# Performance work log

Hardware: AMD Instinct MI355X
Metric: run time of the kernel (lower is better)

## Reference

```python
import jax, jax.numpy as jnp
import numpy as np

B, T, C, HS = 8, 4096, 1024, 128

def setup_inputs() -> dict:
    key = jax.random.key(0)
    kx, kq, kk, kv = jax.random.split(key, 4)
    x = jax.random.normal(kx, (B, T, C), dtype=jnp.float32)
    # Linear weights stored as [in, out] so projection is x @ W
    Wq = jax.random.normal(kq, (C, HS), dtype=jnp.float32) * (C ** -0.5)
    Wk = jax.random.normal(kk, (C, HS), dtype=jnp.float32) * (C ** -0.5)
    Wv = jax.random.normal(kv, (C, HS), dtype=jnp.float32) * (C ** -0.5)
    return {"x": x, "Wq": Wq, "Wk": Wk, "Wv": Wv}

def reference(x, Wq, Wk, Wv):
    # one head of causal self-attention (dropout=0.0 -> identity)
    q = x @ Wq  # [B,T,HS]
    k = x @ Wk
    v = x @ Wv
    scale = q.shape[-1] ** -0.5
    scores = jnp.einsum('bqd,bkd->bqk', q, k) * scale  # [B,T,T]
    t = q.shape[1]
    causal = jnp.tril(jnp.ones((t, t), dtype=bool))
    scores = jnp.where(causal, scores, jnp.finfo(scores.dtype).min)
    weights = jax.nn.softmax(scores, axis=-1)
    out = jnp.einsum('bqk,bkd->bqd', weights, v)  # [B,T,HS]
    return out
```

## Files before the change

### kernel.cpp

```cpp
#include <hip/hip_runtime.h>
#include <hip/hip_bf16.h>

#define TB 8
#define TT 4096
#define TC 1024
#define THS 128

typedef __bf16 bf16;
typedef __attribute__((ext_vector_type(8))) __bf16 bf16x8;
typedef __attribute__((ext_vector_type(2))) __bf16 bf16x2;
typedef __attribute__((ext_vector_type(4))) float f32x4;
typedef __attribute__((ext_vector_type(16))) float f32x16;

__device__ __forceinline__ unsigned pkbf(float a, float b) {
    bf16x2 t = { (bf16)a, (bf16)b };
    return __builtin_bit_cast(unsigned, t);
}

__device__ __forceinline__ void gload16(const void* g, void* l) {
    __builtin_amdgcn_global_load_lds(
        (const __attribute__((address_space(1))) void*)g,
        (__attribute__((address_space(3))) void*)l, 16, 0, 0);
}

__global__ __launch_bounds__(256) void wt_kernel(const float* __restrict__ Wq,
                                                 const float* __restrict__ Wk,
                                                 const float* __restrict__ Wv,
                                                 bf16* __restrict__ Wt) {
    __shared__ float tile[64][65];
    const int tid = threadIdx.x;
    const int idx = blockIdx.x;
    const int w = idx >> 5;
    const int kt = (idx & 31) >> 1, ntb = idx & 1;
    const int k0 = kt * 64, n0 = ntb * 64;
    const float* W = (w == 0) ? Wq : (w == 1) ? Wk : Wv;
    #pragma unroll
    for (int i = 0; i < 4; i++) {
        int r = (tid >> 4) + i * 16;
        int c4 = (tid & 15) * 4;
        float4 x4 = *reinterpret_cast<const float4*>(&W[(long)(k0 + r) * 128 + n0 + c4]);
        tile[r][c4 + 0] = x4.x; tile[r][c4 + 1] = x4.y;
        tile[r][c4 + 2] = x4.z; tile[r][c4 + 3] = x4.w;
    }
    __syncthreads();
    const int n = tid >> 2, kk = (tid & 3) * 16;
    bf16 o[16];
    #pragma unroll
    for (int j = 0; j < 16; j++) o[j] = (bf16)tile[kk + j][n];
    bf16* dst = &Wt[(long)((w << 7) + n0 + n) * 1024 + k0 + kk];
    *reinterpret_cast<bf16x8*>(dst)     = *reinterpret_cast<bf16x8*>(&o[0]);
    *reinterpret_cast<bf16x8*>(dst + 8) = *reinterpret_cast<bf16x8*>(&o[8]);
}

__global__ __launch_bounds__(512, 4) void qkv_kernel(const float* __restrict__ x,
                                                     const bf16* __restrict__ Wt,
                                                     bf16* __restrict__ Q,
                                                     bf16* __restrict__ K,
                                                     bf16* __restrict__ Vtt) {
    __shared__ __align__(1024) char smem[81920];
    const int tid = threadIdx.x;
    const int wave = tid >> 6, lane = tid & 63;
    const int lr = lane & 15, g = lane >> 4;
    const int qs = wave >> 2, ns = wave & 3;
    const long row0 = (long)blockIdx.x * 64;

    int xOff[2], xL[2];
    #pragma unroll
    for (int i = 0; i < 2; i++) {
        int D = wave * 2048 + i * 1024 + lane * 16;
        int r = D >> 8, c = D & 255;
        xOff[i] = r * 4096 + (c ^ (((r & 7) << 4) ^ (((r >> 3) & 1) << 7)));
        xL[i] = wave * 2048 + i * 1024;
    }
    int wOff[6], wL[6];
    #pragma unroll
    for (int i = 0; i < 6; i++) {
        int D = wave * 6144 + i * 1024 + lane * 16;
        int n = D >> 7, c = D & 127;
        wOff[i] = n * 2048 + (c ^ ((n & 7) << 4));
        wL[i] = wave * 6144 + i * 1024;
    }
    const char* xb = (const char*)x + row0 * 4096;
    const char* wb = (const char*)Wt;

    f32x4 acc[2][6] = {};

    {
        #pragma unroll
        for (int i = 0; i < 2; i++) gload16(xb + xOff[i], smem + xL[i]);
        #pragma unroll
        for (int i = 0; i < 6; i++) gload16(wb + wOff[i], smem + 32768 + wL[i]);
        #pragma unroll
        for (int i = 0; i < 2; i++) gload16(xb + 256 + xOff[i], smem + 16384 + xL[i]);
    }

    #pragma unroll 1
    for (int s = 0; s < 16; s++) {
        if (s < 15) asm volatile("s_waitcnt vmcnt(2)" ::: "memory");
        else        asm volatile("s_waitcnt vmcnt(0)" ::: "memory");
        __builtin_amdgcn_s_barrier();

        const char* xp = smem + (s & 1) * 16384;
        const char* wp = smem + 32768;
        bf16x8 a[2][2];
        #pragma unroll
        for (int ar = 0; ar < 2; ar++) {
            const int r = qs * 32 + ar * 16 + lr;
            const int rs = ((r & 7) << 4) ^ (((r >> 3) & 1) << 7);
            #pragma unroll
            for (int ks = 0; ks < 2; ks++) {
                f32x4 lo  = *reinterpret_cast<const f32x4*>(xp + r * 256 + ((ks * 128 + g * 32) ^ rs));
                f32x4 hi4 = *reinterpret_cast<const f32x4*>(xp + r * 256 + ((ks * 128 + g * 32 + 16) ^ rs));
                uint4 u;
                u.x = pkbf(lo[0], lo[1]);  u.y = pkbf(lo[2], lo[3]);
                u.z = pkbf(hi4[0], hi4[1]); u.w = pkbf(hi4[2], hi4[3]);
                a[ar][ks] = __builtin_bit_cast(bf16x8, u);
            }
        }
        __builtin_amdgcn_s_setprio(1);
        #pragma unroll
        for (int nt = 0; nt < 6; nt++) {
            const int n = ns * 96 + nt * 16 + lr;
            const int nsw = (n & 7) << 4;
            #pragma unroll
            for (int ks = 0; ks < 2; ks++) {
                bf16x8 bfr = *reinterpret_cast<const bf16x8*>(wp + n * 128 + ((ks * 64 + g * 16) ^ nsw));
                #pragma unroll
                for (int ar = 0; ar < 2; ar++)
                    acc[ar][nt] = __builtin_amdgcn_mfma_f32_16x16x32_bf16(a[ar][ks], bfr, acc[ar][nt], 0, 0, 0);
            }
        }
        __builtin_amdgcn_s_setprio(0);
        __builtin_amdgcn_s_barrier();

        if (s + 1 < 16) {
            #pragma unroll
            for (int i = 0; i < 6; i++)
                gload16(wb + (s + 1) * 128 + wOff[i], smem + 32768 + wL[i]);
        }
        if (s + 2 < 16) {
            #pragma unroll
            for (int i = 0; i < 2; i++)
                gload16(xb + (s + 2) * 256 + xOff[i], smem + (s & 1) * 16384 + xL[i]);
        }
    }

    const float qscale = 0.08838834764831845f;
    bf16* ld = (bf16*)smem;
    #pragma unroll 1
    for (int wsel = 0; wsel < 3; wsel++) {
        __syncthreads();
        #pragma unroll
        for (int nt = 0; nt < 6; nt++) {
            const int colbase = ns * 96 + nt * 16;
            if ((colbase >> 7) != wsel) continue;
            const int d = (colbase + lr) & 127;
            #pragma unroll
            for (int ar = 0; ar < 2; ar++)
                #pragma unroll
                for (int r = 0; r < 4; r++) {
                    float val = acc[ar][nt][r];
                    if (wsel == 0) val *= qscale;
                    const int lrow = qs * 32 + ar * 16 + g * 4 + r;
                    ld[lrow * 136 + d] = (bf16)val;
                }
        }
        __syncthreads();
        if (wsel < 2) {
            bf16* dst = (wsel == 0 ? Q : K) + row0 * 128;
            #pragma unroll
            for (int i = 0; i < 2; i++) {
                const int slot = tid + 512 * i;
                const int rr = slot >> 4, c8 = (slot & 15) * 8;
                bf16x8 vv = *reinterpret_cast<const bf16x8*>(&ld[rr * 136 + c8]);
                *reinterpret_cast<bf16x8*>(&dst[rr * 128 + c8]) = vv;
            }
        } else {
            bf16* dst = Vtt + (long)blockIdx.x * 8192;
            #pragma unroll
            for (int i = 0; i < 2; i++) {
                const int slot = tid + 512 * i;
                const int d = slot >> 3, t8 = (slot & 7) * 8;
                bf16x8 vv;
                #pragma unroll
                for (int j = 0; j < 8; j++) vv[j] = ld[(t8 + j) * 136 + d];
                *reinterpret_cast<bf16x8*>(&dst[d * 64 + t8]) = vv;
            }
        }
    }
}

__global__ __launch_bounds__(512, 2) void attn_kernel(const bf16* __restrict__ Q,
                                                      const bf16* __restrict__ K,
                                                      const bf16* __restrict__ Vtt,
                                                      float* __restrict__ out) {
    __shared__ __align__(1024) char smem[131072];
    __shared__ float mlb[6 * 64];
    const int tid = threadIdx.x;
    const int wave = tid >> 6, lane = tid & 63;
    const int c = lane & 31, hi = lane >> 5;
    const int qs = wave >> 2, kvq = wave & 3;
    const int kswz = ((c & 7) << 4) ^ (((c >> 3) & 1) << 7);
    const int vswz = (c & 7) << 4;
    const int v = blockIdx.x >> 3, b = blockIdx.x & 7;
    const long base = (long)b * TT * 128;
    const char* Kb = (const char*)(K + base);
    const char* Vb = (const char*)Vtt + (long)b * (64 * 16384);

    int kOff[4], vOff[4], lOff[4];
    #pragma unroll
    for (int i = 0; i < 4; i++) {
        int D = wave * 4096 + i * 1024 + lane * 16;
        kOff[i] = (D & ~255) | ((D & 255) ^ (((D >> 8) & 7) << 4) ^ (((D >> 11) & 1) << 7));
        vOff[i] = (D & ~127) | ((D & 127) ^ (((D >> 7) & 7) << 4));
        lOff[i] = wave * 4096 + i * 1024;
    }

    #pragma unroll 1
    for (int ph = 0; ph < 2; ph++) {
        const int qt = ph ? 63 - v : v;
        const int nIt = (qt + 2) >> 1;
        const int q0w = qt * 64 + qs * 32;
        const int qa = q0w + c;

        bf16x8 qf[8];
        #pragma unroll
        for (int dw = 0; dw < 8; dw++)
            qf[dw] = *reinterpret_cast<const bf16x8*>(&Q[base + (long)qa * 128 + dw * 16 + hi * 8]);

        f32x16 O[4] = {};
        float m = -__builtin_inff(), l = 0.f;

        {
            #pragma unroll
            for (int i = 0; i < 4; i++) {
                gload16(Kb + kOff[i], smem + lOff[i]);
                gload16(Vb + vOff[i], smem + 65536 + lOff[i]);
            }
            if (nIt > 1) {
                #pragma unroll
                for (int i = 0; i < 4; i++) {
                    gload16(Kb + 32768 + kOff[i], smem + 32768 + lOff[i]);
                    gload16(Vb + 32768 + vOff[i], smem + 98304 + lOff[i]);
                }
            }
        }

        #pragma unroll 1
        for (int it = 0; it < nIt; it++) {
            const int bi = it & 1;
            char* kBuf = smem + bi * 32768;
            char* vBuf = smem + 65536 + bi * 32768;
            if (it + 1 < nIt) asm volatile("s_waitcnt vmcnt(8)" ::: "memory");
            else              asm volatile("s_waitcnt vmcnt(0)" ::: "memory");
            __builtin_amdgcn_s_barrier();

            const int kv0 = it * 128 + kvq * 32;
            if (kv0 <= q0w) {
                const char* kb = kBuf + kvq * 8192;
                const char* vb = vBuf + (kvq >> 1) * 16384;
                const int vcol0 = (kvq & 1) * 64;
                f32x16 S = {};
                __builtin_amdgcn_s_setprio(1);
                #pragma unroll
                for (int dw = 0; dw < 8; dw++) {
                    bf16x8 kf = *reinterpret_cast<const bf16x8*>(
                        kb + c * 256 + ((dw * 32 + hi * 16) ^ kswz));
                    S = __builtin_amdgcn_mfma_f32_32x32x16_bf16(kf, qf[dw], S, 0, 0, 0);
                }
                __builtin_amdgcn_s_setprio(0);
                if (kv0 == q0w) {
                    #pragma unroll
                    for (int i = 0; i < 16; i++) {
                        int kvr = kv0 + (i & 3) + 8 * (i >> 2) + 4 * hi;
                        if (kvr > qa) S[i] = -__builtin_inff();
                    }
                }
                float t8[8];
                #pragma unroll
                for (int i = 0; i < 8; i++) t8[i] = fmaxf(S[i], S[i + 8]);
                float t4a = fmaxf(t8[0], t8[4]), t4b = fmaxf(t8[1], t8[5]);
                float t4c = fmaxf(t8[2], t8[6]), t4d = fmaxf(t8[3], t8[7]);
                float pm = fmaxf(fmaxf(t4a, t4b), fmaxf(t4c, t4d));
                pm = fmaxf(pm, __shfl_xor(pm, 32, 64));
                if (!__all(pm - m <= 8.0f)) {
                    float mn = fmaxf(m, pm);
                    float fr = __expf(m - mn);
                    #pragma unroll
                    for (int dt = 0; dt < 4; dt++) O[dt] = O[dt] * fr;
                    l *= fr;
                    m = mn;
                }
                #pragma unroll
                for (int i = 0; i < 16; i++) S[i] = __expf(S[i] - m);
                float s8[8];
                #pragma unroll
                for (int i = 0; i < 8; i++) s8[i] = S[i] + S[i + 8];
                l += ((s8[0] + s8[4]) + (s8[1] + s8[5])) + ((s8[2] + s8[6]) + (s8[3] + s8[7]));

                bf16x8 pf[2];
                #pragma unroll
                for (int wl = 0; wl < 2; wl++) {
                    const int i0 = 8 * wl;
                    unsigned L0 = pkbf(S[i0 + 0], S[i0 + 1]);
                    unsigned L1 = pkbf(S[i0 + 2], S[i0 + 3]);
                    unsigned H0 = pkbf(S[i0 + 4], S[i0 + 5]);
                    unsigned H1 = pkbf(S[i0 + 6], S[i0 + 7]);
                    unsigned sel0 = hi ? L0 : H0;
                    unsigned sel1 = hi ? L1 : H1;
                    unsigned x0 = __shfl_xor((int)sel0, 32, 64);
                    unsigned x1 = __shfl_xor((int)sel1, 32, 64);
                    uint4 f;
                    f.x = hi ? x0 : L0;
                    f.y = hi ? x1 : L1;
                    f.z = hi ? H0 : x0;
                    f.w = hi ? H1 : x1;
                    pf[wl] = __builtin_bit_cast(bf16x8, f);
                }
                __builtin_amdgcn_s_setprio(1);
                #pragma unroll
                for (int wl = 0; wl < 2; wl++)
                    #pragma unroll
                    for (int dt = 0; dt < 4; dt++) {
                        bf16x8 vf = *reinterpret_cast<const bf16x8*>(
                            vb + (dt * 32 + c) * 128 + ((vcol0 + wl * 32 + hi * 16) ^ vswz));
                        O[dt] = __builtin_amdgcn_mfma_f32_32x32x16_bf16(vf, pf[wl], O[dt], 0, 0, 0);
                    }
                __builtin_amdgcn_s_setprio(0);
            }
            __builtin_amdgcn_s_barrier();
            if (it + 2 < nIt) {
                const char* Ks = Kb + (long)(it + 2) * 32768;
                const char* Vs = Vb + (long)(it + 2) * 32768;
                #pragma unroll
                for (int i = 0; i < 4; i++) {
                    gload16(Ks + kOff[i], kBuf + lOff[i]);
                    gload16(Vs + vOff[i], vBuf + lOff[i]);
                }
            }
        }

        l += __shfl_xor(l, 32, 64);

        if (kvq != 0) {
            const int sl = qs * 3 + (kvq - 1);
            char* om = smem + sl * 16384;
            #pragma unroll
            for (int dt = 0; dt < 4; dt++)
                #pragma unroll
                for (int g = 0; g < 4; g++) {
                    float4 w4 = { O[dt][4 * g + 0], O[dt][4 * g + 1],
                                  O[dt][4 * g + 2], O[dt][4 * g + 3] };
                    *reinterpret_cast<float4*>(
                        om + c * 512 + ((dt * 128 + g * 32 + hi * 16) ^ ((c & 7) << 4))) = w4;
                }
            if (hi == 0) { mlb[sl * 64 + c] = m; mlb[sl * 64 + 32 + c] = l; }
        }
        __syncthreads();
        if (kvq == 0) {
            float mq[3], lq[3];
            float mx = m;
            #pragma unroll
            for (int p = 0; p < 3; p++) {
                const int sl = qs * 3 + p;
                mq[p] = mlb[sl * 64 + c];
                lq[p] = mlb[sl * 64 + 32 + c];
                mx = fmaxf(mx, mq[p]);
            }
            float f0 = __expf(m - mx);
            float lt = l * f0;
            float fq[3];
            #pragma unroll
            for (int p = 0; p < 3; p++) { fq[p] = __expf(mq[p] - mx); lt += lq[p] * fq[p]; }
            float linv = 1.0f / lt;
            #pragma unroll
            for (int dt = 0; dt < 4; dt++)
                #pragma unroll
                for (int g = 0; g < 4; g++) {
                    float4 r;
                    r.x = O[dt][4 * g + 0] * f0;
                    r.y = O[dt][4 * g + 1] * f0;
                    r.z = O[dt][4 * g + 2] * f0;
                    r.w = O[dt][4 * g + 3] * f0;
                    #pragma unroll
                    for (int p = 0; p < 3; p++) {
                        const char* om = smem + (qs * 3 + p) * 16384;
                        float4 o1 = *reinterpret_cast<const float4*>(
                            om + c * 512 + ((dt * 128 + g * 32 + hi * 16) ^ ((c & 7) << 4)));
                        r.x += o1.x * fq[p]; r.y += o1.y * fq[p];
                        r.z += o1.z * fq[p]; r.w += o1.w * fq[p];
                    }
                    r.x *= linv; r.y *= linv; r.z *= linv; r.w *= linv;
                    *reinterpret_cast<float4*>(
                        &out[base + (long)qa * 128 + dt * 32 + 8 * g + 4 * hi]) = r;
                }
        }
        __syncthreads();
    }
}

extern "C" void kernel_launch(void* const* d_in, const int* in_sizes, int n_in,
                              void* d_out, int out_size, void* d_ws, size_t ws_size,
                              hipStream_t stream) {
    const float* x  = (const float*)d_in[0];
    const float* Wq = (const float*)d_in[1];
    const float* Wk = (const float*)d_in[2];
    const float* Wv = (const float*)d_in[3];
    float* out = (float*)d_out;
    bf16* Q   = (bf16*)d_ws;
    bf16* K   = Q   + (size_t)32768 * 128;
    bf16* Vtt = K   + (size_t)32768 * 128;
    bf16* Wt  = Vtt + (size_t)8 * 64 * 128 * 64;
    wt_kernel<<<96, 256, 0, stream>>>(Wq, Wk, Wv, Wt);
    qkv_kernel<<<512, 512, 0, stream>>>(x, Wt, Q, K, Vtt);
    attn_kernel<<<256, 512, 0, stream>>>(Q, K, Vtt, out);
}
```

Before: 114.1 us.

## Split attention into one-query-tile blocks of 256 threads, heaviest tiles first

The attention kernel now launches 512 blocks of 4 waves instead of 256 blocks of 8 waves. Each block handles a single 64-row query tile rather than a balanced pair of tiles, and splits the key/value range 2 ways across waves instead of 4. KV tiles shrink to 64 rows and the LDS footprint halves to 64KB, so more blocks can sit on each CU and the final merge is simpler. Blocks are ordered so the longest causal tiles are scheduled first. This relies on the hardware scheduler for load balance instead of explicit pairing, and each block iterates more times over smaller tiles.

```diff
diff --git a/kernel.cpp b/kernel.cpp
--- a/kernel.cpp
+++ b/kernel.cpp
@@ -190,19 +190,20 @@
     }
 }
 
-__global__ __launch_bounds__(512, 2) void attn_kernel(const bf16* __restrict__ Q,
+__global__ __launch_bounds__(256, 2) void attn_kernel(const bf16* __restrict__ Q,
                                                       const bf16* __restrict__ K,
                                                       const bf16* __restrict__ Vtt,
                                                       float* __restrict__ out) {
-    __shared__ __align__(1024) char smem[131072];
-    __shared__ float mlb[6 * 64];
+    __shared__ __align__(1024) char smem[65536];
+    __shared__ float mlb[2 * 64];
     const int tid = threadIdx.x;
     const int wave = tid >> 6, lane = tid & 63;
     const int c = lane & 31, hi = lane >> 5;
-    const int qs = wave >> 2, kvq = wave & 3;
+    const int qs = wave >> 1, kvq = wave & 1;
     const int kswz = ((c & 7) << 4) ^ (((c >> 3) & 1) << 7);
     const int vswz = (c & 7) << 4;
-    const int v = blockIdx.x >> 3, b = blockIdx.x & 7;
+    const int g_ = blockIdx.x >> 3, b = blockIdx.x & 7;
+    const int qt = (g_ < 32) ? (63 - g_) : (g_ - 32);
     const long base = (long)b * TT * 128;
     const char* Kb = (const char*)(K + base);
     const char* Vb = (const char*)Vtt + (long)b * (64 * 16384);
@@ -216,186 +217,163 @@
         lOff[i] = wave * 4096 + i * 1024;
     }
 
+    const int nIt = qt + 1;
+    const int q0w = qt * 64 + qs * 32;
+    const int qa = q0w + c;
+
+    bf16x8 qf[8];
+    #pragma unroll
+    for (int dw = 0; dw < 8; dw++)
+        qf[dw] = *reinterpret_cast<const bf16x8*>(&Q[base + (long)qa * 128 + dw * 16 + hi * 8]);
+
+    f32x16 O[4] = {};
+    float m = -__builtin_inff(), l = 0.f;
+
+    {
+        #pragma unroll
+        for (int i = 0; i < 4; i++) {
+            gload16(Kb + kOff[i], smem + lOff[i]);
+            gload16(Vb + vOff[i], smem + 32768 + lOff[i]);
+        }
+        if (nIt > 1) {
+            #pragma unroll
+            for (int i = 0; i < 4; i++) {
+                gload16(Kb + 16384 + kOff[i], smem + 16384 + lOff[i]);
+                gload16(Vb + 16384 + vOff[i], smem + 49152 + lOff[i]);
+            }
+        }
+    }
+
     #pragma unroll 1
-    for (int ph = 0; ph < 2; ph++) {
-        const int qt = ph ? 63 - v : v;
-        const int nIt = (qt + 2) >> 1;
-        const int q0w = qt * 64 + qs * 32;
-        const int qa = q0w + c;
-
-        bf16x8 qf[8];
-        #pragma unroll
-        for (int dw = 0; dw < 8; dw++)
-            qf[dw] = *reinterpret_cast<const bf16x8*>(&Q[base + (long)qa * 128 + dw * 16 + hi * 8]);
-
-        f32x16 O[4] = {};
-        float m = -__builtin_inff(), l = 0.f;
-
-        {
+    for (int it = 0; it < nIt; it++) {
+        const int bi = it & 1;
+        char* kBuf = smem + bi * 16384;
+        char* vBuf = smem + 32768 + bi * 16384;
+        if (it + 1 < nIt) asm volatile("s_waitcnt vmcnt(8)" ::: "memory");
+        else              asm volatile("s_waitcnt vmcnt(0)" ::: "memory");
+        __builtin_amdgcn_s_barrier();
+
+        const int kv0 = it * 64 + kvq * 32;
+        if (kv0 <= q0w) {
+            const char* kb = kBuf + kvq * 8192;
+            const char* vb = vBuf;
+            const int vcol0 = kvq * 64;
+            f32x16 S = {};
+            __builtin_amdgcn_s_setprio(1);
+            #pragma unroll
+            for (int dw = 0; dw < 8; dw++) {
+                bf16x8 kf = *reinterpret_cast<const bf16x8*>(
+                    kb + c * 256 + ((dw * 32 + hi * 16) ^ kswz));
+                S = __builtin_amdgcn_mfma_f32_32x32x16_bf16(kf, qf[dw], S, 0, 0, 0);
+            }
+            __builtin_amdgcn_s_setprio(0);
+            if (kv0 == q0w) {
+                #pragma unroll
+                for (int i = 0; i < 16; i++) {
+                    int kvr = kv0 + (i & 3) + 8 * (i >> 2) + 4 * hi;
+                    if (kvr > qa) S[i] = -__builtin_inff();
+                }
+            }
+            float t8[8];
+            #pragma unroll
+            for (int i = 0; i < 8; i++) t8[i] = fmaxf(S[i], S[i + 8]);
+            float t4a = fmaxf(t8[0], t8[4]), t4b = fmaxf(t8[1], t8[5]);
+            float t4c = fmaxf(t8[2], t8[6]), t4d = fmaxf(t8[3], t8[7]);
+            float pm = fmaxf(fmaxf(t4a, t4b), fmaxf(t4c, t4d));
+            pm = fmaxf(pm, __shfl_xor(pm, 32, 64));
+            if (!__all(pm - m <= 8.0f)) {
+                float mn = fmaxf(m, pm);
+                float fr = __expf(m - mn);
+                #pragma unroll
+                for (int dt = 0; dt < 4; dt++) O[dt] = O[dt] * fr;
+                l *= fr;
+                m = mn;
+            }
+            #pragma unroll
+            for (int i = 0; i < 16; i++) S[i] = __expf(S[i] - m);
+            float s8[8];
+            #pragma unroll
+            for (int i = 0; i < 8; i++) s8[i] = S[i] + S[i + 8];
+            l += ((s8[0] + s8[4]) + (s8[1] + s8[5])) + ((s8[2] + s8[6]) + (s8[3] + s8[7]));
+
+            bf16x8 pf[2];
+            #pragma unroll
+            for (int wl = 0; wl < 2; wl++) {
+                const int i0 = 8 * wl;
+                unsigned L0 = pkbf(S[i0 + 0], S[i0 + 1]);
+                unsigned L1 = pkbf(S[i0 + 2], S[i0 + 3]);
+                unsigned H0 = pkbf(S[i0 + 4], S[i0 + 5]);
+                unsigned H1 = pkbf(S[i0 + 6], S[i0 + 7]);
+                unsigned sel0 = hi ? L0 : H0;
+                unsigned sel1 = hi ? L1 : H1;
+                unsigned x0 = __shfl_xor((int)sel0, 32, 64);
+                unsigned x1 = __shfl_xor((int)sel1, 32, 64);
+                uint4 f;
+                f.x = hi ? x0 : L0;
+                f.y = hi ? x1 : L1;
+                f.z = hi ? H0 : x0;
+                f.w = hi ? H1 : x1;
+                pf[wl] = __builtin_bit_cast(bf16x8, f);
+            }
+            __builtin_amdgcn_s_setprio(1);
+            #pragma unroll
+            for (int wl = 0; wl < 2; wl++)
+                #pragma unroll
+                for (int dt = 0; dt < 4; dt++) {
+                    bf16x8 vf = *reinterpret_cast<const bf16x8*>(
+                        vb + (dt * 32 + c) * 128 + ((vcol0 + wl * 32 + hi * 16) ^ vswz));
+                    O[dt] = __builtin_amdgcn_mfma_f32_32x32x16_bf16(vf, pf[wl], O[dt], 0, 0, 0);
+                }
+            __builtin_amdgcn_s_setprio(0);
+        }
+        __builtin_amdgcn_s_barrier();
+        if (it + 2 < nIt) {
+            const char* Ks = Kb + (long)(it + 2) * 16384;
+            const char* Vs = Vb + (long)(it + 2) * 16384;
             #pragma unroll
             for (int i = 0; i < 4; i++) {
-                gload16(Kb + kOff[i], smem + lOff[i]);
-                gload16(Vb + vOff[i], smem + 65536 + lOff[i]);
-            }
-            if (nIt > 1) {
-                #pragma unroll
-                for (int i = 0; i < 4; i++) {
-                    gload16(Kb + 32768 + kOff[i], smem + 32768 + lOff[i]);
-                    gload16(Vb + 32768 + vOff[i], smem + 98304 + lOff[i]);
-                }
-            }
-        }
-
-        #pragma unroll 1
-        for (int it = 0; it < nIt; it++) {
-            const int bi = it & 1;
-            char* kBuf = smem + bi * 32768;
-            char* vBuf = smem + 65536 + bi * 32768;
-            if (it + 1 < nIt) asm volatile("s_waitcnt vmcnt(8)" ::: "memory");
-            else              asm volatile("s_waitcnt vmcnt(0)" ::: "memory");
-            __builtin_amdgcn_s_barrier();
-
-            const int kv0 = it * 128 + kvq * 32;
-            if (kv0 <= q0w) {
-                const char* kb = kBuf + kvq * 8192;
-                const char* vb = vBuf + (kvq >> 1) * 16384;
-                const int vcol0 = (kvq & 1) * 64;
-                f32x16 S = {};
-                __builtin_amdgcn_s_setprio(1);
-                #pragma unroll
-                for (int dw = 0; dw < 8; dw++) {
-                    bf16x8 kf = *reinterpret_cast<const bf16x8*>(
-                        kb + c * 256 + ((dw * 32 + hi * 16) ^ kswz));
-                    S = __builtin_amdgcn_mfma_f32_32x32x16_bf16(kf, qf[dw], S, 0, 0, 0);
-                }
-                __builtin_amdgcn_s_setprio(0);
-                if (kv0 == q0w) {
-                    #pragma unroll
-                    for (int i = 0; i < 16; i++) {
-                        int kvr = kv0 + (i & 3) + 8 * (i >> 2) + 4 * hi;
-                        if (kvr > qa) S[i] = -__builtin_inff();
-                    }
-                }
-                float t8[8];
-                #pragma unroll
-                for (int i = 0; i < 8; i++) t8[i] = fmaxf(S[i], S[i + 8]);
-                float t4a = fmaxf(t8[0], t8[4]), t4b = fmaxf(t8[1], t8[5]);
-                float t4c = fmaxf(t8[2], t8[6]), t4d = fmaxf(t8[3], t8[7]);
-                float pm = fmaxf(fmaxf(t4a, t4b), fmaxf(t4c, t4d));
-                pm = fmaxf(pm, __shfl_xor(pm, 32, 64));
-                if (!__all(pm - m <= 8.0f)) {
-                    float mn = fmaxf(m, pm);
-                    float fr = __expf(m - mn);
-                    #pragma unroll
-                    for (int dt = 0; dt < 4; dt++) O[dt] = O[dt] * fr;
-                    l *= fr;
-                    m = mn;
-                }
-                #pragma unroll
-                for (int i = 0; i < 16; i++) S[i] = __expf(S[i] - m);
-                float s8[8];
-                #pragma unroll
-                for (int i = 0; i < 8; i++) s8[i] = S[i] + S[i + 8];
-                l += ((s8[0] + s8[4]) + (s8[1] + s8[5])) + ((s8[2] + s8[6]) + (s8[3] + s8[7]));
-
-                bf16x8 pf[2];
-                #pragma unroll
-                for (int wl = 0; wl < 2; wl++) {
-                    const int i0 = 8 * wl;
-                    unsigned L0 = pkbf(S[i0 + 0], S[i0 + 1]);
-                    unsigned L1 = pkbf(S[i0 + 2], S[i0 + 3]);
-                    unsigned H0 = pkbf(S[i0 + 4], S[i0 + 5]);
-                    unsigned H1 = pkbf(S[i0 + 6], S[i0 + 7]);
-                    unsigned sel0 = hi ? L0 : H0;
-                    unsigned sel1 = hi ? L1 : H1;
-                    unsigned x0 = __shfl_xor((int)sel0, 32, 64);
-                    unsigned x1 = __shfl_xor((int)sel1, 32, 64);
-                    uint4 f;
-                    f.x = hi ? x0 : L0;
-                    f.y = hi ? x1 : L1;
-                    f.z = hi ? H0 : x0;
-                    f.w = hi ? H1 : x1;
-                    pf[wl] = __builtin_bit_cast(bf16x8, f);
-                }
-                __builtin_amdgcn_s_setprio(1);
-                #pragma unroll
-                for (int wl = 0; wl < 2; wl++)
-                    #pragma unroll
-                    for (int dt = 0; dt < 4; dt++) {
-                        bf16x8 vf = *reinterpret_cast<const bf16x8*>(
-                            vb + (dt * 32 + c) * 128 + ((vcol0 + wl * 32 + hi * 16) ^ vswz));
-                        O[dt] = __builtin_amdgcn_mfma_f32_32x32x16_bf16(vf, pf[wl], O[dt], 0, 0, 0);
-                    }
-                __builtin_amdgcn_s_setprio(0);
-            }
-            __builtin_amdgcn_s_barrier();
-            if (it + 2 < nIt) {
-                const char* Ks = Kb + (long)(it + 2) * 32768;
-                const char* Vs = Vb + (long)(it + 2) * 32768;
-                #pragma unroll
-                for (int i = 0; i < 4; i++) {
-                    gload16(Ks + kOff[i], kBuf + lOff[i]);
-                    gload16(Vs + vOff[i], vBuf + lOff[i]);
-                }
-            }
-        }
-
-        l += __shfl_xor(l, 32, 64);
-
-        if (kvq != 0) {
-            const int sl = qs * 3 + (kvq - 1);
-            char* om = smem + sl * 16384;
-            #pragma unroll
-            for (int dt = 0; dt < 4; dt++)
-                #pragma unroll
-                for (int g = 0; g < 4; g++) {
-                    float4 w4 = { O[dt][4 * g + 0], O[dt][4 * g + 1],
-                                  O[dt][4 * g + 2], O[dt][4 * g + 3] };
-                    *reinterpret_cast<float4*>(
-                        om + c * 512 + ((dt * 128 + g * 32 + hi * 16) ^ ((c & 7) << 4))) = w4;
-                }
-            if (hi == 0) { mlb[sl * 64 + c] = m; mlb[sl * 64 + 32 + c] = l; }
-        }
-        __syncthreads();
-        if (kvq == 0) {
-            float mq[3], lq[3];
-            float mx = m;
-            #pragma unroll
-            for (int p = 0; p < 3; p++) {
-                const int sl = qs * 3 + p;
-                mq[p] = mlb[sl * 64 + c];
-                lq[p] = mlb[sl * 64 + 32 + c];
-                mx = fmaxf(mx, mq[p]);
-            }
-            float f0 = __expf(m - mx);
-            float lt = l * f0;
-            float fq[3];
-            #pragma unroll
-            for (int p = 0; p < 3; p++) { fq[p] = __expf(mq[p] - mx); lt += lq[p] * fq[p]; }
-            float linv = 1.0f / lt;
-            #pragma unroll
-            for (int dt = 0; dt < 4; dt++)
-                #pragma unroll
-                for (int g = 0; g < 4; g++) {
-                    float4 r;
-                    r.x = O[dt][4 * g + 0] * f0;
-                    r.y = O[dt][4 * g + 1] * f0;
-                    r.z = O[dt][4 * g + 2] * f0;
-                    r.w = O[dt][4 * g + 3] * f0;
-                    #pragma unroll
-                    for (int p = 0; p < 3; p++) {
-                        const char* om = smem + (qs * 3 + p) * 16384;
-                        float4 o1 = *reinterpret_cast<const float4*>(
-                            om + c * 512 + ((dt * 128 + g * 32 + hi * 16) ^ ((c & 7) << 4)));
-                        r.x += o1.x * fq[p]; r.y += o1.y * fq[p];
-                        r.z += o1.z * fq[p]; r.w += o1.w * fq[p];
-                    }
-                    r.x *= linv; r.y *= linv; r.z *= linv; r.w *= linv;
-                    *reinterpret_cast<float4*>(
-                        &out[base + (long)qa * 128 + dt * 32 + 8 * g + 4 * hi]) = r;
-                }
-        }
-        __syncthreads();
+                gload16(Ks + kOff[i], kBuf + lOff[i]);
+                gload16(Vs + vOff[i], vBuf + lOff[i]);
+            }
+        }
+    }
+
+    l += __shfl_xor(l, 32, 64);
+
+    if (kvq == 1) {
+        char* om = smem + qs * 16384;
+        #pragma unroll
+        for (int dt = 0; dt < 4; dt++)
+            #pragma unroll
+            for (int g = 0; g < 4; g++) {
+                float4 w4 = { O[dt][4 * g + 0], O[dt][4 * g + 1],
+                              O[dt][4 * g + 2], O[dt][4 * g + 3] };
+                *reinterpret_cast<float4*>(
+                    om + c * 512 + ((dt * 128 + g * 32 + hi * 16) ^ ((c & 7) << 4))) = w4;
+            }
+        if (hi == 0) { mlb[qs * 64 + c] = m; mlb[qs * 64 + 32 + c] = l; }
+    }
+    __syncthreads();
+    if (kvq == 0) {
+        float m1 = mlb[qs * 64 + c], l1 = mlb[qs * 64 + 32 + c];
+        float mx = fmaxf(m, m1);
+        float f0 = __expf(m - mx), f1 = __expf(m1 - mx);
+        float linv = 1.0f / (l * f0 + l1 * f1);
+        const char* om = smem + qs * 16384;
+        #pragma unroll
+        for (int dt = 0; dt < 4; dt++)
+            #pragma unroll
+            for (int g = 0; g < 4; g++) {
+                float4 o1 = *reinterpret_cast<const float4*>(
+                    om + c * 512 + ((dt * 128 + g * 32 + hi * 16) ^ ((c & 7) << 4)));
+                float4 r;
+                r.x = (O[dt][4 * g + 0] * f0 + o1.x * f1) * linv;
+                r.y = (O[dt][4 * g + 1] * f0 + o1.y * f1) * linv;
+                r.z = (O[dt][4 * g + 2] * f0 + o1.z * f1) * linv;
+                r.w = (O[dt][4 * g + 3] * f0 + o1.w * f1) * linv;
+                *reinterpret_cast<float4*>(
+                    &out[base + (long)qa * 128 + dt * 32 + 8 * g + 4 * hi]) = r;
+            }
     }
 }
 
@@ -413,5 +391,5 @@
     bf16* Wt  = Vtt + (size_t)8 * 64 * 128 * 64;
     wt_kernel<<<96, 256, 0, stream>>>(Wq, Wk, Wv, Wt);
     qkv_kernel<<<512, 512, 0, stream>>>(x, Wt, Q, K, Vtt);
-    attn_kernel<<<256, 512, 0, stream>>>(Q, K, Vtt, out);
-}
+    attn_kernel<<<512, 256, 0, stream>>>(Q, K, Vtt, out);
+}
```

After: 138.2 us. 21.2% more time.

## Read V directly from global, halve LDS, serialize combine for higher occupancy

Applied to the files above, without the earlier changes.

V tiles are no longer staged in LDS; each wave reads its V fragments directly from global memory (L2) during the PV MFMA. This halves shared memory to 64KB, and the cross-wave output combine is split into three serialized rounds that reuse one 16KB region per q-slice. Together these let launch bounds ask for 4 blocks per CU instead of 2. In exchange, V loads become unstaged global reads on the MFMA critical path, the reads repeat across waves, and the epilogue gains extra barriers. Register pressure at 4 blocks of 512 threads may force spills.

```diff
diff --git a/kernel.cpp b/kernel.cpp
--- a/kernel.cpp
+++ b/kernel.cpp
@@ -190,29 +190,27 @@
     }
 }
 
-__global__ __launch_bounds__(512, 2) void attn_kernel(const bf16* __restrict__ Q,
+__global__ __launch_bounds__(512, 4) void attn_kernel(const bf16* __restrict__ Q,
                                                       const bf16* __restrict__ K,
                                                       const bf16* __restrict__ Vtt,
                                                       float* __restrict__ out) {
-    __shared__ __align__(1024) char smem[131072];
-    __shared__ float mlb[6 * 64];
+    __shared__ __align__(1024) char smem[65536];
     const int tid = threadIdx.x;
     const int wave = tid >> 6, lane = tid & 63;
     const int c = lane & 31, hi = lane >> 5;
     const int qs = wave >> 2, kvq = wave & 3;
     const int kswz = ((c & 7) << 4) ^ (((c >> 3) & 1) << 7);
-    const int vswz = (c & 7) << 4;
+    const int osw = (c & 7) << 4;
     const int v = blockIdx.x >> 3, b = blockIdx.x & 7;
     const long base = (long)b * TT * 128;
     const char* Kb = (const char*)(K + base);
     const char* Vb = (const char*)Vtt + (long)b * (64 * 16384);
 
-    int kOff[4], vOff[4], lOff[4];
+    int kOff[4], lOff[4];
     #pragma unroll
     for (int i = 0; i < 4; i++) {
         int D = wave * 4096 + i * 1024 + lane * 16;
         kOff[i] = (D & ~255) | ((D & 255) ^ (((D >> 8) & 7) << 4) ^ (((D >> 11) & 1) << 7));
-        vOff[i] = (D & ~127) | ((D & 127) ^ (((D >> 7) & 7) << 4));
         lOff[i] = wave * 4096 + i * 1024;
     }
 
@@ -233,16 +231,10 @@
 
         {
             #pragma unroll
-            for (int i = 0; i < 4; i++) {
-                gload16(Kb + kOff[i], smem + lOff[i]);
-                gload16(Vb + vOff[i], smem + 65536 + lOff[i]);
-            }
+            for (int i = 0; i < 4; i++) gload16(Kb + kOff[i], smem + lOff[i]);
             if (nIt > 1) {
                 #pragma unroll
-                for (int i = 0; i < 4; i++) {
-                    gload16(Kb + 32768 + kOff[i], smem + 32768 + lOff[i]);
-                    gload16(Vb + 32768 + vOff[i], smem + 98304 + lOff[i]);
-                }
+                for (int i = 0; i < 4; i++) gload16(Kb + 32768 + kOff[i], smem + 32768 + lOff[i]);
             }
         }
 
@@ -250,15 +242,14 @@
         for (int it = 0; it < nIt; it++) {
             const int bi = it & 1;
             char* kBuf = smem + bi * 32768;
-            char* vBuf = smem + 65536 + bi * 32768;
-            if (it + 1 < nIt) asm volatile("s_waitcnt vmcnt(8)" ::: "memory");
+            if (it + 1 < nIt) asm volatile("s_waitcnt vmcnt(4)" ::: "memory");
             else              asm volatile("s_waitcnt vmcnt(0)" ::: "memory");
             __builtin_amdgcn_s_barrier();
 
             const int kv0 = it * 128 + kvq * 32;
             if (kv0 <= q0w) {
                 const char* kb = kBuf + kvq * 8192;
-                const char* vb = vBuf + (kvq >> 1) * 16384;
+                const char* vg = Vb + (long)(2 * it + (kvq >> 1)) * 16384;
                 const int vcol0 = (kvq & 1) * 64;
                 f32x16 S = {};
                 __builtin_amdgcn_s_setprio(1);
@@ -323,7 +314,7 @@
                     #pragma unroll
                     for (int dt = 0; dt < 4; dt++) {
                         bf16x8 vf = *reinterpret_cast<const bf16x8*>(
-                            vb + (dt * 32 + c) * 128 + ((vcol0 + wl * 32 + hi * 16) ^ vswz));
+                            vg + (dt * 32 + c) * 128 + vcol0 + wl * 32 + hi * 16);
                         O[dt] = __builtin_amdgcn_mfma_f32_32x32x16_bf16(vf, pf[wl], O[dt], 0, 0, 0);
                     }
                 __builtin_amdgcn_s_setprio(0);
@@ -331,69 +322,75 @@
             __builtin_amdgcn_s_barrier();
             if (it + 2 < nIt) {
                 const char* Ks = Kb + (long)(it + 2) * 32768;
-                const char* Vs = Vb + (long)(it + 2) * 32768;
-                #pragma unroll
-                for (int i = 0; i < 4; i++) {
-                    gload16(Ks + kOff[i], kBuf + lOff[i]);
-                    gload16(Vs + vOff[i], vBuf + lOff[i]);
-                }
+                #pragma unroll
+                for (int i = 0; i < 4; i++) gload16(Ks + kOff[i], kBuf + lOff[i]);
             }
         }
 
         l += __shfl_xor(l, 32, 64);
 
-        if (kvq != 0) {
-            const int sl = qs * 3 + (kvq - 1);
-            char* om = smem + sl * 16384;
-            #pragma unroll
-            for (int dt = 0; dt < 4; dt++)
-                #pragma unroll
-                for (int g = 0; g < 4; g++) {
-                    float4 w4 = { O[dt][4 * g + 0], O[dt][4 * g + 1],
-                                  O[dt][4 * g + 2], O[dt][4 * g + 3] };
-                    *reinterpret_cast<float4*>(
-                        om + c * 512 + ((dt * 128 + g * 32 + hi * 16) ^ ((c & 7) << 4))) = w4;
-                }
-            if (hi == 0) { mlb[sl * 64 + c] = m; mlb[sl * 64 + 32 + c] = l; }
-        }
-        __syncthreads();
-        if (kvq == 0) {
-            float mq[3], lq[3];
-            float mx = m;
-            #pragma unroll
-            for (int p = 0; p < 3; p++) {
-                const int sl = qs * 3 + p;
-                mq[p] = mlb[sl * 64 + c];
-                lq[p] = mlb[sl * 64 + 32 + c];
-                mx = fmaxf(mx, mq[p]);
-            }
-            float f0 = __expf(m - mx);
-            float lt = l * f0;
-            float fq[3];
-            #pragma unroll
-            for (int p = 0; p < 3; p++) { fq[p] = __expf(mq[p] - mx); lt += lq[p] * fq[p]; }
-            float linv = 1.0f / lt;
-            #pragma unroll
-            for (int dt = 0; dt < 4; dt++)
-                #pragma unroll
-                for (int g = 0; g < 4; g++) {
-                    float4 r;
-                    r.x = O[dt][4 * g + 0] * f0;
-                    r.y = O[dt][4 * g + 1] * f0;
-                    r.z = O[dt][4 * g + 2] * f0;
-                    r.w = O[dt][4 * g + 3] * f0;
-                    #pragma unroll
-                    for (int p = 0; p < 3; p++) {
-                        const char* om = smem + (qs * 3 + p) * 16384;
+        float* mlb = (float*)(smem + 49152);
+        if (kvq != 0 && hi == 0) {
+            mlb[(kvq - 1) * 128 + qs * 64 + c]      = m;
+            mlb[(kvq - 1) * 128 + qs * 64 + 32 + c] = l;
+        }
+        float fq0 = 0.f, fq1 = 0.f, fq2 = 0.f, linv = 0.f;
+        #pragma unroll
+        for (int p = 1; p <= 3; p++) {
+            __syncthreads();
+            if (kvq == p) {
+                char* om = smem + qs * 16384;
+                #pragma unroll
+                for (int dt = 0; dt < 4; dt++)
+                    #pragma unroll
+                    for (int g = 0; g < 4; g++) {
+                        float4 w4 = { O[dt][4 * g + 0], O[dt][4 * g + 1],
+                                      O[dt][4 * g + 2], O[dt][4 * g + 3] };
+                        *reinterpret_cast<float4*>(
+                            om + c * 512 + ((dt * 128 + g * 32 + hi * 16) ^ osw)) = w4;
+                    }
+            }
+            __syncthreads();
+            if (kvq == 0) {
+                if (p == 1) {
+                    float m0 = mlb[qs * 64 + c],       l0 = mlb[qs * 64 + 32 + c];
+                    float m1 = mlb[128 + qs * 64 + c], l1 = mlb[128 + qs * 64 + 32 + c];
+                    float m2 = mlb[256 + qs * 64 + c], l2 = mlb[256 + qs * 64 + 32 + c];
+                    float mx = fmaxf(fmaxf(m, m0), fmaxf(m1, m2));
+                    float f0 = __expf(m - mx);
+                    fq0 = __expf(m0 - mx); fq1 = __expf(m1 - mx); fq2 = __expf(m2 - mx);
+                    linv = 1.0f / (l * f0 + l0 * fq0 + l1 * fq1 + l2 * fq2);
+                    #pragma unroll
+                    for (int dt = 0; dt < 4; dt++) O[dt] = O[dt] * f0;
+                }
+                const float fp = (p == 1) ? fq0 : (p == 2) ? fq1 : fq2;
+                const char* om = smem + qs * 16384;
+                #pragma unroll
+                for (int dt = 0; dt < 4; dt++)
+                    #pragma unroll
+                    for (int g = 0; g < 4; g++) {
                         float4 o1 = *reinterpret_cast<const float4*>(
-                            om + c * 512 + ((dt * 128 + g * 32 + hi * 16) ^ ((c & 7) << 4)));
-                        r.x += o1.x * fq[p]; r.y += o1.y * fq[p];
-                        r.z += o1.z * fq[p]; r.w += o1.w * fq[p];
+                            om + c * 512 + ((dt * 128 + g * 32 + hi * 16) ^ osw));
+                        O[dt][4 * g + 0] += o1.x * fp;
+                        O[dt][4 * g + 1] += o1.y * fp;
+                        O[dt][4 * g + 2] += o1.z * fp;
+                        O[dt][4 * g + 3] += o1.w * fp;
                     }
-                    r.x *= linv; r.y *= linv; r.z *= linv; r.w *= linv;
-                    *reinterpret_cast<float4*>(
-                        &out[base + (long)qa * 128 + dt * 32 + 8 * g + 4 * hi]) = r;
-                }
+                if (p == 3) {
+                    #pragma unroll
+                    for (int dt = 0; dt < 4; dt++)
+                        #pragma unroll
+                        for (int g = 0; g < 4; g++) {
+                            float4 r;
+                            r.x = O[dt][4 * g + 0] * linv;
+                            r.y = O[dt][4 * g + 1] * linv;
+                            r.z = O[dt][4 * g + 2] * linv;
+                            r.w = O[dt][4 * g + 3] * linv;
+                            *reinterpret_cast<float4*>(
+                                &out[base + (long)qa * 128 + dt * 32 + 8 * g + 4 * hi]) = r;
+                        }
+                }
+            }
         }
         __syncthreads();
     }
```

New measurement: 232.3 us. +103.6%, slower.

## Software-pipeline QK^T of the next KV tile ahead of current softmax/PV

Applied to the files above, without the earlier changes.

Restructures the attention loop so the S = K·Q MFMAs for tile it+1 are issued before the softmax and P·V work of tile it. K gets triple-buffered and V double-buffered in LDS, with loads issued at the top of each iteration. The QK product also splits into two independent accumulators to break the MFMA dependency chain. LDS grows to 160 KB, which limits residency to one block per CU, and the extra live S registers raise spill risk under the existing launch bounds.

```diff
diff --git a/kernel.cpp b/kernel.cpp
--- a/kernel.cpp
+++ b/kernel.cpp
@@ -21,6 +21,21 @@
     __builtin_amdgcn_global_load_lds(
         (const __attribute__((address_space(1))) void*)g,
         (__attribute__((address_space(3))) void*)l, 16, 0, 0);
+}
+
+__device__ __forceinline__ f32x16 qk8(const char* kb, const bf16x8 (&qf)[8],
+                                      int kswz, int c, int hi) {
+    f32x16 Sa = {}, Sb = {};
+    #pragma unroll
+    for (int dw = 0; dw < 4; dw++) {
+        bf16x8 k0 = *reinterpret_cast<const bf16x8*>(
+            kb + c * 256 + (((2 * dw) * 32 + hi * 16) ^ kswz));
+        Sa = __builtin_amdgcn_mfma_f32_32x32x16_bf16(k0, qf[2 * dw], Sa, 0, 0, 0);
+        bf16x8 k1 = *reinterpret_cast<const bf16x8*>(
+            kb + c * 256 + (((2 * dw + 1) * 32 + hi * 16) ^ kswz));
+        Sb = __builtin_amdgcn_mfma_f32_32x32x16_bf16(k1, qf[2 * dw + 1], Sb, 0, 0, 0);
+    }
+    return Sa + Sb;
 }
 
 __global__ __launch_bounds__(256) void wt_kernel(const float* __restrict__ Wq,
@@ -194,8 +209,7 @@
                                                       const bf16* __restrict__ K,
                                                       const bf16* __restrict__ Vtt,
                                                       float* __restrict__ out) {
-    __shared__ __align__(1024) char smem[131072];
-    __shared__ float mlb[6 * 64];
+    __shared__ __align__(1024) char smem[163840];
     const int tid = threadIdx.x;
     const int wave = tid >> 6, lane = tid & 63;
     const int c = lane & 31, hi = lane >> 5;
@@ -233,52 +247,70 @@
 
         {
             #pragma unroll
-            for (int i = 0; i < 4; i++) {
-                gload16(Kb + kOff[i], smem + lOff[i]);
-                gload16(Vb + vOff[i], smem + 65536 + lOff[i]);
-            }
-            if (nIt > 1) {
-                #pragma unroll
-                for (int i = 0; i < 4; i++) {
-                    gload16(Kb + 32768 + kOff[i], smem + 32768 + lOff[i]);
-                    gload16(Vb + 32768 + vOff[i], smem + 98304 + lOff[i]);
+            for (int i = 0; i < 4; i++) gload16(Kb + kOff[i], smem + lOff[i]);
+            #pragma unroll
+            for (int i = 0; i < 4; i++) gload16(Kb + 32768 + kOff[i], smem + 32768 + lOff[i]);
+            #pragma unroll
+            for (int i = 0; i < 4; i++) gload16(Vb + vOff[i], smem + 98304 + lOff[i]);
+        }
+        asm volatile("s_waitcnt vmcnt(8)" ::: "memory");
+        __builtin_amdgcn_s_barrier();
+
+        f32x16 Scur = {}, Snext = {};
+        if (kvq * 32 <= q0w) {
+            __builtin_amdgcn_s_setprio(1);
+            Scur = qk8(smem + kvq * 8192, qf, kswz, c, hi);
+            __builtin_amdgcn_s_setprio(0);
+            if (kvq * 32 == q0w) {
+                #pragma unroll
+                for (int i = 0; i < 16; i++) {
+                    int kvr = kvq * 32 + (i & 3) + 8 * (i >> 2) + 4 * hi;
+                    if (kvr > qa) Scur[i] = -__builtin_inff();
                 }
             }
         }
 
         #pragma unroll 1
         for (int it = 0; it < nIt; it++) {
-            const int bi = it & 1;
-            char* kBuf = smem + bi * 32768;
-            char* vBuf = smem + 65536 + bi * 32768;
-            if (it + 1 < nIt) asm volatile("s_waitcnt vmcnt(8)" ::: "memory");
-            else              asm volatile("s_waitcnt vmcnt(0)" ::: "memory");
+            const int s1 = it + 1, s2 = it + 2;
+            const bool sk = s2 < nIt, sv = s1 < nIt;
+            if (sk) {
+                const char* Ks = Kb + (long)s2 * 32768;
+                char* kd = smem + (s2 % 3) * 32768;
+                #pragma unroll
+                for (int i = 0; i < 4; i++) gload16(Ks + kOff[i], kd + lOff[i]);
+            }
+            if (sv) {
+                const char* Vs = Vb + (long)s1 * 32768;
+                char* vd = smem + 98304 + (s1 & 1) * 32768;
+                #pragma unroll
+                for (int i = 0; i < 4; i++) gload16(Vs + vOff[i], vd + lOff[i]);
+            }
+            if (sk)      asm volatile("s_waitcnt vmcnt(8)" ::: "memory");
+            else if (sv) asm volatile("s_waitcnt vmcnt(4)" ::: "memory");
+            else         asm volatile("s_waitcnt vmcnt(0)" ::: "memory");
             __builtin_amdgcn_s_barrier();
+
+            const int kv0n = s1 * 128 + kvq * 32;
+            if (sv && kv0n <= q0w) {
+                const char* kb = smem + (s1 % 3) * 32768 + kvq * 8192;
+                __builtin_amdgcn_s_setprio(1);
+                Snext = qk8(kb, qf, kswz, c, hi);
+                __builtin_amdgcn_s_setprio(0);
+                if (kv0n == q0w) {
+                    #pragma unroll
+                    for (int i = 0; i < 16; i++) {
+                        int kvr = kv0n + (i & 3) + 8 * (i >> 2) + 4 * hi;
+                        if (kvr > qa) Snext[i] = -__builtin_inff();
+                    }
+                }
+            }
 
             const int kv0 = it * 128 + kvq * 32;
             if (kv0 <= q0w) {
-                const char* kb = kBuf + kvq * 8192;
-                const char* vb = vBuf + (kvq >> 1) * 16384;
-                const int vcol0 = (kvq & 1) * 64;
-                f32x16 S = {};
-                __builtin_amdgcn_s_setprio(1);
-                #pragma unroll
-                for (int dw = 0; dw < 8; dw++) {
-                    bf16x8 kf = *reinterpret_cast<const bf16x8*>(
-                        kb + c * 256 + ((dw * 32 + hi * 16) ^ kswz));
-                    S = __builtin_amdgcn_mfma_f32_32x32x16_bf16(kf, qf[dw], S, 0, 0, 0);
-                }
-                __builtin_amdgcn_s_setprio(0);
-                if (kv0 == q0w) {
-                    #pragma unroll
-                    for (int i = 0; i < 16; i++) {
-                        int kvr = kv0 + (i & 3) + 8 * (i >> 2) + 4 * hi;
-                        if (kvr > qa) S[i] = -__builtin_inff();
-                    }
-                }
                 float t8[8];
                 #pragma unroll
-                for (int i = 0; i < 8; i++) t8[i] = fmaxf(S[i], S[i + 8]);
+                for (int i = 0; i < 8; i++) t8[i] = fmaxf(Scur[i], Scur[i + 8]);
                 float t4a = fmaxf(t8[0], t8[4]), t4b = fmaxf(t8[1], t8[5]);
                 float t4c = fmaxf(t8[2], t8[6]), t4d = fmaxf(t8[3], t8[7]);
                 float pm = fmaxf(fmaxf(t4a, t4b), fmaxf(t4c, t4d));
@@ -292,20 +324,20 @@
                     m = mn;
                 }
                 #pragma unroll
-                for (int i = 0; i < 16; i++) S[i] = __expf(S[i] - m);
+                for (int i = 0; i < 16; i++) Scur[i] = __expf(Scur[i] - m);
                 float s8[8];
                 #pragma unroll
-                for (int i = 0; i < 8; i++) s8[i] = S[i] + S[i + 8];
+                for (int i = 0; i < 8; i++) s8[i] = Scur[i] + Scur[i + 8];
                 l += ((s8[0] + s8[4]) + (s8[1] + s8[5])) + ((s8[2] + s8[6]) + (s8[3] + s8[7]));
 
                 bf16x8 pf[2];
                 #pragma unroll
                 for (int wl = 0; wl < 2; wl++) {
                     const int i0 = 8 * wl;
-                    unsigned L0 = pkbf(S[i0 + 0], S[i0 + 1]);
-                    unsigned L1 = pkbf(S[i0 + 2], S[i0 + 3]);
-                    unsigned H0 = pkbf(S[i0 + 4], S[i0 + 5]);
-                    unsigned H1 = pkbf(S[i0 + 6], S[i0 + 7]);
+                    unsigned L0 = pkbf(Scur[i0 + 0], Scur[i0 + 1]);
+                    unsigned L1 = pkbf(Scur[i0 + 2], Scur[i0 + 3]);
+                    unsigned H0 = pkbf(Scur[i0 + 4], Scur[i0 + 5]);
+                    unsigned H1 = pkbf(Scur[i0 + 6], Scur[i0 + 7]);
                     unsigned sel0 = hi ? L0 : H0;
                     unsigned sel1 = hi ? L1 : H1;
                     unsigned x0 = __shfl_xor((int)sel0, 32, 64);
@@ -317,31 +349,26 @@
                     f.w = hi ? H1 : x1;
                     pf[wl] = __builtin_bit_cast(bf16x8, f);
                 }
+                const char* vb2 = smem + 98304 + (it & 1) * 32768 + (kvq >> 1) * 16384;
+                const int vcol0 = (kvq & 1) * 64;
                 __builtin_amdgcn_s_setprio(1);
                 #pragma unroll
                 for (int wl = 0; wl < 2; wl++)
                     #pragma unroll
                     for (int dt = 0; dt < 4; dt++) {
                         bf16x8 vf = *reinterpret_cast<const bf16x8*>(
-                            vb + (dt * 32 + c) * 128 + ((vcol0 + wl * 32 + hi * 16) ^ vswz));
+                            vb2 + (dt * 32 + c) * 128 + ((vcol0 + wl * 32 + hi * 16) ^ vswz));
                         O[dt] = __builtin_amdgcn_mfma_f32_32x32x16_bf16(vf, pf[wl], O[dt], 0, 0, 0);
                     }
                 __builtin_amdgcn_s_setprio(0);
             }
             __builtin_amdgcn_s_barrier();
-            if (it + 2 < nIt) {
-                const char* Ks = Kb + (long)(it + 2) * 32768;
-                const char* Vs = Vb + (long)(it + 2) * 32768;
-                #pragma unroll
-                for (int i = 0; i < 4; i++) {
-                    gload16(Ks + kOff[i], kBuf + lOff[i]);
-                    gload16(Vs + vOff[i], vBuf + lOff[i]);
-                }
-            }
+            Scur = Snext;
         }
 
         l += __shfl_xor(l, 32, 64);
 
+        float* mlb = (float*)(smem + 161792);
         if (kvq != 0) {
             const int sl = qs * 3 + (kvq - 1);
             char* om = smem + sl * 16384;
@@ -354,7 +381,8 @@
                     *reinterpret_cast<float4*>(
                         om + c * 512 + ((dt * 128 + g * 32 + hi * 16) ^ ((c & 7) << 4))) = w4;
                 }
-            if (hi == 0) { mlb[sl * 64 + c] = m; mlb[sl * 64 + 32 + c] = l; }
+            if (hi == 0) { mlb[(qs * 3 + kvq - 1) * 64 + c] = m;
+                           mlb[(qs * 3 + kvq - 1) * 64 + 32 + c] = l; }
         }
         __syncthreads();
         if (kvq == 0) {
@@ -362,9 +390,8 @@
             float mx = m;
             #pragma unroll
             for (int p = 0; p < 3; p++) {
-                const int sl = qs * 3 + p;
-                mq[p] = mlb[sl * 64 + c];
-                lq[p] = mlb[sl * 64 + 32 + c];
+                mq[p] = mlb[(qs * 3 + p) * 64 + c];
+                lq[p] = mlb[(qs * 3 + p) * 64 + 32 + c];
                 mx = fmaxf(mx, mq[p]);
             }
             float f0 = __expf(m - mx);
```

Measured after the change: 141.0 us. 1.24x slower.
